# Kernel tuning notes

Hardware: AMD Instinct MI355X
Metric: run time of the kernel (lower is better)

Reference implementation:

```python
import jax, jax.numpy as jnp
import numpy as np

B, S, D, H, O, E = 2, 2048, 1024, 2048, 1024, 8


def setup_inputs() -> dict:
    key = jax.random.key(0)
    k_x, k_rw, k_w1, k_w3, k_w2 = jax.random.split(key, 5)
    sD = 1.0 / np.sqrt(D)
    sH = 1.0 / np.sqrt(H)
    return {
        "x": jax.random.normal(k_x, (B, S, D), dtype=jnp.float32),
        "router_w": jax.random.normal(k_rw, (E, D), dtype=jnp.float32) * sD,  # nn.Linear(D, E).weight
        "router_b": jnp.zeros((E,), dtype=jnp.float32),
        "W1": jax.random.normal(k_w1, (E, D, H), dtype=jnp.float32) * sD,  # per-expert w1 (x @ W1)
        "W3": jax.random.normal(k_w3, (E, D, H), dtype=jnp.float32) * sD,  # per-expert gate w3
        "W2": jax.random.normal(k_w2, (E, H, O), dtype=jnp.float32) * sH,  # per-expert down-proj
        "top_k": 2,
    }


def reference(x, router_w, router_b, W1, W3, W2, top_k):
    b, s, d = x.shape
    xf = x.reshape(-1, d)  # [T, D], T = B*S
    T = xf.shape[0]

    # Router: softmax over experts, then top-k and renormalize
    logits = xf @ router_w.T + router_b            # [T, E]
    probs = jax.nn.softmax(logits, axis=-1)
    top_p, top_i = jax.lax.top_k(probs, top_k)     # [T, k]
    top_p = top_p / top_p.sum(axis=-1, keepdims=True)

    # Dense all-expert SwiGLU MLPs (faithful to reference: every expert on every token)
    h = jnp.einsum('td,edh->eth', xf, W1)          # [E, T, H]
    g = jnp.einsum('td,edh->eth', xf, W3)          # [E, T, H]
    eo = jnp.einsum('eth,eho->eto', jax.nn.silu(h) * g, W2)  # [E, T, O]

    # Gather each token's top-k expert outputs and combine
    sel = eo[top_i, jnp.arange(T)[:, None]]        # [T, k, O]
    out = jnp.sum(top_p[..., None] * sel, axis=1)  # [T, O]
    return out.reshape(b, s, -1)
```

## Files before the change

kernel.cpp:

```cpp
#include <hip/hip_runtime.h>
#include <hip/hip_bf16.h>

#define TTOK 4096
#define DIM  1024
#define HID  2048
#define ODIM 1024
#define NE   8

typedef __attribute__((ext_vector_type(8))) short  short8;
typedef __attribute__((ext_vector_type(4))) float  f32x4;
typedef __attribute__((ext_vector_type(8))) unsigned short ushort8;

#define WAITVM(N) asm volatile("s_waitcnt vmcnt(" #N ")" ::: "memory")
#define BAR() __builtin_amdgcn_s_barrier()

__device__ __forceinline__ unsigned short f2bf(float f){
  unsigned u = __float_as_uint(f);
  u += 0x7fffu + ((u >> 16) & 1u);
  return (unsigned short)(u >> 16);
}

__device__ __forceinline__ void gld16(const void* g, void* l){
  __builtin_amdgcn_global_load_lds(
      (const __attribute__((address_space(1))) unsigned int*)g,
      (__attribute__((address_space(3))) unsigned int*)l, 16, 0, 0);
}

__global__ __launch_bounds__(256) void router_kernel(
    const float* __restrict__ x, const float* __restrict__ rw,
    const float* __restrict__ rb, unsigned short* __restrict__ xbf,
    int2* __restrict__ toke, float2* __restrict__ tokw)
{
  int tok  = (blockIdx.x * blockDim.x + threadIdx.x) >> 6;
  int lane = threadIdx.x & 63;
  const float4* xr = (const float4*)(x + (size_t)tok * DIM + lane * 16);
  float xv[16];
#pragma unroll
  for (int q = 0; q < 4; q++){
    float4 v = xr[q];
    xv[q*4+0]=v.x; xv[q*4+1]=v.y; xv[q*4+2]=v.z; xv[q*4+3]=v.w;
  }
  ushort8 u0, u1;
#pragma unroll
  for (int j = 0; j < 8; j++){ u0[j] = f2bf(xv[j]); u1[j] = f2bf(xv[8+j]); }
  ushort8* xo = (ushort8*)(xbf + (size_t)tok * DIM + lane * 16);
  xo[0] = u0; xo[1] = u1;

  float lg[NE];
#pragma unroll
  for (int e = 0; e < NE; e++){
    const float4* wr4 = (const float4*)(rw + (size_t)e * DIM + lane * 16);
    float s = 0.f;
#pragma unroll
    for (int q = 0; q < 4; q++){
      float4 wv = wr4[q];
      s += xv[q*4+0]*wv.x + xv[q*4+1]*wv.y + xv[q*4+2]*wv.z + xv[q*4+3]*wv.w;
    }
    lg[e] = s;
  }
#pragma unroll
  for (int e = 0; e < NE; e++)
    for (int s = 1; s < 64; s <<= 1) lg[e] += __shfl_xor(lg[e], s, 64);

  if (lane == 0){
#pragma unroll
    for (int e = 0; e < NE; e++) lg[e] += rb[e];
    int e0 = 0; float l0 = lg[0];
    for (int e = 1; e < NE; e++) if (lg[e] > l0){ l0 = lg[e]; e0 = e; }
    int e1 = -1; float l1 = -1e30f;
    for (int e = 0; e < NE; e++) if (e != e0 && lg[e] > l1){ l1 = lg[e]; e1 = e; }
    float w0 = 1.f / (1.f + __expf(l1 - l0));
    float w1 = 1.f / (1.f + __expf(l0 - l1));
    toke[tok] = make_int2(e0, e1);
    tokw[tok] = make_float2(w0, w1);
  }
}

__global__ __launch_bounds__(256) void plan_kernel(
    const int2* __restrict__ toke, const float2* __restrict__ tokw,
    int* __restrict__ counts, int* __restrict__ offs,
    int* __restrict__ tlist, float* __restrict__ wlist)
{
  const int e  = blockIdx.x;
  const int t  = threadIdx.x;
  const int lane = t & 63, wv = t >> 6;
  __shared__ int sh[4 * 8];
  __shared__ int tot[8];
  __shared__ int sw[4];

  int wcnt[NE];
#pragma unroll
  for (int ee = 0; ee < NE; ee++) wcnt[ee] = 0;
  for (int base = 0; base < TTOK; base += 256){
    int2 p = toke[base + t];
#pragma unroll
    for (int ee = 0; ee < NE; ee++){
      unsigned long long m = __ballot(p.x == ee || p.y == ee);
      if (lane == 0) wcnt[ee] += __popcll(m);
    }
  }
  if (lane == 0){
#pragma unroll
    for (int ee = 0; ee < NE; ee++) sh[wv * 8 + ee] = wcnt[ee];
  }
  __syncthreads();
  if (t < NE) tot[t] = sh[t] + sh[8 + t] + sh[16 + t] + sh[24 + t];
  __syncthreads();

  int my_off = 0;
#pragma unroll
  for (int ee = 0; ee < NE; ee++) if (ee < e) my_off += tot[ee];

  if (e == 0 && t < NE){
    counts[t] = tot[t];
    int o = 0;
    for (int ee = 0; ee < NE; ee++){ if (ee < t) o += tot[ee]; }
    offs[t] = o;
    if (t == 0){
      int s = 0;
      for (int ee = 0; ee < NE; ee++) s += tot[ee];
      offs[NE] = s;
    }
  }

  int running = my_off;
  for (int base = 0; base < TTOK; base += 256){
    int tokid = base + t;
    int2  p = toke[tokid];
    float2 wgt = tokw[tokid];
    bool s0 = (p.x == e), s1 = (p.y == e);
    bool flag = s0 || s1;
    unsigned long long m = __ballot(flag);
    int rank_in_wave = __popcll(m & ((lane == 0) ? 0ull : ((~0ull) >> (64 - lane))));
    if (lane == 0) sw[wv] = __popcll(m);
    __syncthreads();
    int wave_base = 0, tot4 = 0;
#pragma unroll
    for (int w2 = 0; w2 < 4; w2++){ int v = sw[w2]; tot4 += v; if (w2 < wv) wave_base += v; }
    if (flag){
      int pos = running + wave_base + rank_in_wave;
      tlist[pos] = tokid;
      wlist[pos] = s0 ? wgt.x : wgt.y;
    }
    running += tot4;
    __syncthreads();
  }
}

__global__ __launch_bounds__(256) void transpose_cvt(
    const float* __restrict__ in, unsigned short* __restrict__ out, int R, int C)
{
  __shared__ __align__(16) unsigned short tl[64 * 128];
  int e = blockIdx.z;
  const float* src = in + (size_t)e * R * C + (size_t)(blockIdx.y * 128) * C + blockIdx.x * 64;
  unsigned short* dst = out + (size_t)e * C * R + (size_t)(blockIdx.x * 64) * R + blockIdx.y * 128;
  int t = threadIdx.x;
#pragma unroll
  for (int i = 0; i < 8; i++){
    int idx = i * 256 + t;
    int c = idx & 63, r0 = (idx >> 6) * 4;
    unsigned short v[4];
#pragma unroll
    for (int j = 0; j < 4; j++) v[j] = f2bf(src[(size_t)(r0 + j) * C + c]);
    unsigned long long pk = (unsigned long long)v[0] | ((unsigned long long)v[1] << 16)
      | ((unsigned long long)v[2] << 32) | ((unsigned long long)v[3] << 48);
    *(unsigned long long*)((char*)tl + c * 256 + (((r0 >> 3) ^ (c & 15)) * 16) + (r0 & 7) * 2) = pk;
  }
  __syncthreads();
#pragma unroll
  for (int i = 0; i < 4; i++){
    int idx = i * 256 + t;
    int c = idx >> 4, r0 = (idx & 15) * 8;
    ushort8 u = *(const ushort8*)((const char*)tl + c * 256 + (((r0 >> 3) ^ (c & 15)) * 16));
    *(ushort8*)(dst + (size_t)c * R + r0) = u;
  }
}

__global__ __launch_bounds__(256,2) void ffn1_kernel(
    const unsigned short* __restrict__ xbf,
    const unsigned short* __restrict__ w1t,
    const unsigned short* __restrict__ w3t,
    unsigned short* __restrict__ abuf,
    const int* __restrict__ counts, const int* __restrict__ offs,
    const int* __restrict__ tlist)
{
  const int wgid = blockIdx.x;
  const int e = wgid & 7;
  const int j = wgid >> 3;
  const int u = j & 15, g = j >> 4;
  const int ct = (g & 7) * 2 + (u >> 3);
  const int rt = (g >> 3) * 8 + (u & 7);
  const int cnt = counts[e];
  const int rbase = rt * 128;
  if (rbase >= cnt) return;
  const int off = offs[e];
  const int rows_left = cnt - rbase;
  const int t = threadIdx.x;
  const int lane = t & 63, w = t >> 6;
  const int wr = w >> 1, wc = w & 1;

  __shared__ __align__(16) unsigned short lds[2 * 12288];

  int ar0 = t >> 2, ar1 = 64 + (t >> 2);
  int psw = (t & 3) ^ ((t >> 3) & 3);
  int ra0 = ar0 < rows_left ? ar0 : rows_left - 1;
  int ra1 = ar1 < rows_left ? ar1 : rows_left - 1;
  int tok0 = tlist[off + rbase + ra0];
  int tok1 = tlist[off + rbase + ra1];
  const char* sA0  = (const char*)xbf + ((size_t)tok0 * DIM) * 2 + psw * 16;
  const char* sA1  = (const char*)xbf + ((size_t)tok1 * DIM) * 2 + psw * 16;
  const char* sB10 = (const char*)w1t + (((size_t)e * HID + ct * 128 + ar0) * DIM) * 2 + psw * 16;
  const char* sB11 = (const char*)w1t + (((size_t)e * HID + ct * 128 + ar1) * DIM) * 2 + psw * 16;
  const char* sB30 = (const char*)w3t + (((size_t)e * HID + ct * 128 + ar0) * DIM) * 2 + psw * 16;
  const char* sB31 = (const char*)w3t + (((size_t)e * HID + ct * 128 + ar1) * DIM) * 2 + psw * 16;
  const int dofs = w * 1024;

  auto STAGE = [&](int bs, int kt){
    int kb = kt << 6;
    char* base = (char*)lds + bs * 24576;
    gld16(sA0  + kb, base +            dofs);
    gld16(sA1  + kb, base +  4096 +    dofs);
    gld16(sB10 + kb, base +  8192 +    dofs);
    gld16(sB11 + kb, base + 12288 +    dofs);
    gld16(sB30 + kb, base + 16384 +    dofs);
    gld16(sB31 + kb, base + 20480 +    dofs);
  };

  const int chsw = ((lane >> 4) ^ ((lane >> 1) & 3)) * 8;
  int aofs[4], b1ofs[4], b3ofs[4];
#pragma unroll
  for (int i = 0; i < 4; i++){
    int am = wr * 64 + i * 16 + (lane & 15);
    int bn = wc * 64 + i * 16 + (lane & 15);
    aofs[i]  = am * 32 + chsw;
    b1ofs[i] = 4096 + bn * 32 + chsw;
    b3ofs[i] = 8192 + bn * 32 + chsw;
  }

  f32x4 acch[4][4], accg[4][4];
#pragma unroll
  for (int i = 0; i < 4; i++)
#pragma unroll
    for (int jj = 0; jj < 4; jj++){
      acch[i][jj] = (f32x4){0.f,0.f,0.f,0.f};
      accg[i][jj] = (f32x4){0.f,0.f,0.f,0.f};
    }

  auto COMPUTE = [&](int bs){
    const unsigned short* L = lds + bs * 12288;
    short8 a[4], b1[4], b3[4];
#pragma unroll
    for (int i = 0; i < 4; i++){
      a[i]  = *(const short8*)(L + aofs[i]);
      b1[i] = *(const short8*)(L + b1ofs[i]);
      b3[i] = *(const short8*)(L + b3ofs[i]);
    }
    __builtin_amdgcn_s_setprio(1);
#pragma unroll
    for (int mi = 0; mi < 4; mi++)
#pragma unroll
      for (int ni = 0; ni < 4; ni++){
        acch[mi][ni] = __builtin_amdgcn_mfma_f32_16x16x32_bf16(a[mi], b1[ni], acch[mi][ni], 0, 0, 0);
        accg[mi][ni] = __builtin_amdgcn_mfma_f32_16x16x32_bf16(a[mi], b3[ni], accg[mi][ni], 0, 0, 0);
      }
    __builtin_amdgcn_s_setprio(0);
  };

  STAGE(0, 0);
  int kt = 0;
  for (; kt < DIM / 32 - 1; ++kt){
    STAGE((kt + 1) & 1, kt + 1);
    WAITVM(6); BAR();
    COMPUTE(kt & 1);
    BAR();
  }
  WAITVM(0); BAR();
  COMPUTE(kt & 1);

#pragma unroll
  for (int mi = 0; mi < 4; mi++)
#pragma unroll
    for (int r = 0; r < 4; r++){
      int row_local = wr * 64 + mi * 16 + ((lane >> 4) << 2) + r;
      if (row_local < rows_left){
        size_t pair = (size_t)(off + rbase + row_local);
        unsigned short* arow = abuf + pair * HID + ct * 128 + wc * 64 + (lane & 15);
#pragma unroll
        for (int ni = 0; ni < 4; ni++){
          float h = acch[mi][ni][r], gg = accg[mi][ni][r];
          float sv = h / (1.f + __expf(-h));
          arow[ni * 16] = f2bf(sv * gg);
        }
      }
    }
}

__global__ __launch_bounds__(256,3) void ffn2_kernel(
    const unsigned short* __restrict__ abuf,
    const unsigned short* __restrict__ w2t,
    float* __restrict__ dout,
    const int* __restrict__ counts, const int* __restrict__ offs,
    const int* __restrict__ tlist, const float* __restrict__ wlist)
{
  const int wgid = blockIdx.x;
  const int e = wgid & 7;
  const int j = wgid >> 3;
  const int u = j & 7, g = j >> 3;
  const int ct = (g & 3) * 2 + (u >> 2);
  const int rt = (g >> 2) * 4 + (u & 3);
  const int cnt = counts[e];
  const int rbase = rt * 128;
  if (rbase >= cnt) return;
  const int off = offs[e];
  const int rows_left = cnt - rbase;
  const int t = threadIdx.x;
  const int lane = t & 63, w = t >> 6;
  const int wr = w >> 1, wc = w & 1;

  __shared__ __align__(16) unsigned short lds[2 * 8192];

  int ar0 = t >> 2, ar1 = 64 + (t >> 2);
  int psw = (t & 3) ^ ((t >> 3) & 3);
  int ra0 = ar0 < rows_left ? ar0 : rows_left - 1;
  int ra1 = ar1 < rows_left ? ar1 : rows_left - 1;
  const char* sA0 = (const char*)abuf + ((size_t)(off + rbase + ra0) * HID) * 2 + psw * 16;
  const char* sA1 = (const char*)abuf + ((size_t)(off + rbase + ra1) * HID) * 2 + psw * 16;
  const char* sB0 = (const char*)w2t + (((size_t)e * ODIM + ct * 128 + ar0) * HID) * 2 + psw * 16;
  const char* sB1 = (const char*)w2t + (((size_t)e * ODIM + ct * 128 + ar1) * HID) * 2 + psw * 16;
  const int dofs = w * 1024;

  auto STAGE = [&](int bs, int kt){
    int kb = kt << 6;
    char* base = (char*)lds + bs * 16384;
    gld16(sA0 + kb, base +           dofs);
    gld16(sA1 + kb, base +  4096 +   dofs);
    gld16(sB0 + kb, base +  8192 +   dofs);
    gld16(sB1 + kb, base + 12288 +   dofs);
  };

  const int chsw = ((lane >> 4) ^ ((lane >> 1) & 3)) * 8;
  int aofs[4], bofs[4];
#pragma unroll
  for (int i = 0; i < 4; i++){
    int am = wr * 64 + i * 16 + (lane & 15);
    int bn = wc * 64 + i * 16 + (lane & 15);
    aofs[i] = am * 32 + chsw;
    bofs[i] = 4096 + bn * 32 + chsw;
  }

  f32x4 acc[4][4];
#pragma unroll
  for (int i = 0; i < 4; i++)
#pragma unroll
    for (int jj = 0; jj < 4; jj++) acc[i][jj] = (f32x4){0.f,0.f,0.f,0.f};

  auto COMPUTE = [&](int bs){
    const unsigned short* L = lds + bs * 8192;
    short8 a[4], b[4];
#pragma unroll
    for (int i = 0; i < 4; i++){
      a[i] = *(const short8*)(L + aofs[i]);
      b[i] = *(const short8*)(L + bofs[i]);
    }
    __builtin_amdgcn_s_setprio(1);
#pragma unroll
    for (int mi = 0; mi < 4; mi++)
#pragma unroll
      for (int ni = 0; ni < 4; ni++)
        acc[mi][ni] = __builtin_amdgcn_mfma_f32_16x16x32_bf16(a[mi], b[ni], acc[mi][ni], 0, 0, 0);
    __builtin_amdgcn_s_setprio(0);
  };

  STAGE(0, 0);
  int kt = 0;
  for (; kt < HID / 32 - 1; ++kt){
    STAGE((kt + 1) & 1, kt + 1);
    WAITVM(4); BAR();
    COMPUTE(kt & 1);
    BAR();
  }
  WAITVM(0); BAR();
  COMPUTE(kt & 1);

#pragma unroll
  for (int mi = 0; mi < 4; mi++)
#pragma unroll
    for (int r = 0; r < 4; r++){
      int row_local = wr * 64 + mi * 16 + ((lane >> 4) << 2) + r;
      if (row_local < rows_left){
        int pair = off + rbase + row_local;
        int token = tlist[pair];
        float p   = wlist[pair];
        float* orow = dout + (size_t)token * ODIM + ct * 128 + wc * 64 + (lane & 15);
#pragma unroll
        for (int ni = 0; ni < 4; ni++)
          atomicAdd(orow + ni * 16, p * acc[mi][ni][r]);
      }
    }
}

extern "C" void kernel_launch(void* const* d_in, const int* in_sizes, int n_in,
                              void* d_out, int out_size, void* d_ws, size_t ws_size,
                              hipStream_t stream)
{
  const float* x  = (const float*)d_in[0];
  const float* rw = (const float*)d_in[1];
  const float* rb = (const float*)d_in[2];
  const float* W1 = (const float*)d_in[3];
  const float* W3 = (const float*)d_in[4];
  const float* W2 = (const float*)d_in[5];

  char* ws = (char*)d_ws;
  const size_t off_ctrl = 0;
  const size_t off_toke = 256;
  const size_t off_tokw = off_toke + (size_t)TTOK * 8;
  const size_t off_tl   = off_tokw + (size_t)TTOK * 8;
  const size_t off_wl   = off_tl   + (size_t)2 * TTOK * 4;
  const size_t off_xbf  = off_wl   + (size_t)2 * TTOK * 4;
  const size_t off_w1t  = off_xbf  + (size_t)TTOK * DIM * 2;
  const size_t off_w3t  = off_w1t  + (size_t)NE * HID * DIM * 2;
  const size_t off_w2t  = off_w3t  + (size_t)NE * HID * DIM * 2;
  const size_t off_ab   = off_w2t  + (size_t)NE * ODIM * HID * 2;
  const size_t need     = off_ab   + (size_t)2 * TTOK * HID * 2;
  if (ws_size < need) return;

  int* counts = (int*)(ws + off_ctrl);
  int* offs   = (int*)(ws + off_ctrl + 64);
  int2*   toke = (int2*)  (ws + off_toke);
  float2* tokw = (float2*)(ws + off_tokw);
  int*    tl   = (int*)   (ws + off_tl);
  float*  wl   = (float*) (ws + off_wl);
  unsigned short* xbf = (unsigned short*)(ws + off_xbf);
  unsigned short* w1t = (unsigned short*)(ws + off_w1t);
  unsigned short* w3t = (unsigned short*)(ws + off_w3t);
  unsigned short* w2t = (unsigned short*)(ws + off_w2t);
  unsigned short* ab  = (unsigned short*)(ws + off_ab);

  hipMemsetAsync(d_out, 0, (size_t)out_size * sizeof(float), stream);

  router_kernel<<<TTOK / 4, 256, 0, stream>>>(x, rw, rb, xbf, toke, tokw);
  plan_kernel<<<NE, 256, 0, stream>>>(toke, tokw, counts, offs, tl, wl);

  transpose_cvt<<<dim3(HID / 64, DIM / 128, NE), 256, 0, stream>>>(W1, w1t, DIM, HID);
  transpose_cvt<<<dim3(HID / 64, DIM / 128, NE), 256, 0, stream>>>(W3, w3t, DIM, HID);
  transpose_cvt<<<dim3(ODIM / 64, HID / 128, NE), 256, 0, stream>>>(W2, w2t, HID, ODIM);

  ffn1_kernel<<<NE * 16 * 32, 256, 0, stream>>>(xbf, w1t, w3t, ab, counts, offs, tl);
  ffn2_kernel<<<NE * 8 * 32, 256, 0, stream>>>(ab, w2t, (float*)d_out, counts, offs, tl, wl);
}
```

Measured before the change: 262.5 us.

## Interleave W1/W3 weights and enlarge FFN GEMM tiles to 256x256 with 8 waves

W1 and W3 are transposed into one interleaved buffer (16-column groups alternating), so the gate and up projections run as a single GEMM with one B operand stream. Both FFN kernels move from 128x128 tiles with 4 waves to 256x256 tiles with 8 waves, a K step of 64 split into two halves, and a finer-grained LDS double-buffer schedule that interleaves loads with half-tile MFMA batches. The aim is more data reuse per LDS load and fewer redundant A reads. In exchange it uses 128KB of LDS per block and more accumulator registers, and the larger tiles leave fewer blocks and coarser padding for the uneven per-expert token counts.

```diff
diff --git a/kernel.cpp b/kernel.cpp
--- a/kernel.cpp
+++ b/kernel.cpp
@@ -148,12 +148,12 @@
 }
 
 __global__ __launch_bounds__(256) void transpose_cvt(
-    const float* __restrict__ in, unsigned short* __restrict__ out, int R, int C)
+    const float* __restrict__ in, unsigned short* __restrict__ out,
+    int R, int C, int ilv, size_t ostride)
 {
   __shared__ __align__(16) unsigned short tl[64 * 128];
   int e = blockIdx.z;
   const float* src = in + (size_t)e * R * C + (size_t)(blockIdx.y * 128) * C + blockIdx.x * 64;
-  unsigned short* dst = out + (size_t)e * C * R + (size_t)(blockIdx.x * 64) * R + blockIdx.y * 128;
   int t = threadIdx.x;
 #pragma unroll
   for (int i = 0; i < 8; i++){
@@ -172,14 +172,16 @@
     int idx = i * 256 + t;
     int c = idx >> 4, r0 = (idx & 15) * 8;
     ushort8 u = *(const ushort8*)((const char*)tl + c * 256 + (((r0 >> 3) ^ (c & 15)) * 16));
-    *(ushort8*)(dst + (size_t)c * R + r0) = u;
-  }
-}
-
-__global__ __launch_bounds__(256,2) void ffn1_kernel(
+    int cg = blockIdx.x * 64 + c;
+    int q  = (ilv < 0) ? cg : (((cg >> 4) << 5) + ilv + (cg & 15));
+    *(ushort8*)(out + (size_t)e * ostride + (size_t)q * R + blockIdx.y * 128 + r0) = u;
+  }
+}
+
+
+__global__ __launch_bounds__(512,2) void ffn1_kernel(
     const unsigned short* __restrict__ xbf,
-    const unsigned short* __restrict__ w1t,
-    const unsigned short* __restrict__ w3t,
+    const unsigned short* __restrict__ wcat,
     unsigned short* __restrict__ abuf,
     const int* __restrict__ counts, const int* __restrict__ offs,
     const int* __restrict__ tlist)
@@ -187,115 +189,109 @@
   const int wgid = blockIdx.x;
   const int e = wgid & 7;
   const int j = wgid >> 3;
-  const int u = j & 15, g = j >> 4;
-  const int ct = (g & 7) * 2 + (u >> 3);
-  const int rt = (g >> 3) * 8 + (u & 7);
+  const int ct = j & 15;
+  const int rt = j >> 4;
   const int cnt = counts[e];
-  const int rbase = rt * 128;
+  const int rbase = rt * 256;
   if (rbase >= cnt) return;
   const int off = offs[e];
   const int rows_left = cnt - rbase;
   const int t = threadIdx.x;
-  const int lane = t & 63, w = t >> 6;
-  const int wr = w >> 1, wc = w & 1;
-
-  __shared__ __align__(16) unsigned short lds[2 * 12288];
-
-  int ar0 = t >> 2, ar1 = 64 + (t >> 2);
-  int psw = (t & 3) ^ ((t >> 3) & 3);
-  int ra0 = ar0 < rows_left ? ar0 : rows_left - 1;
-  int ra1 = ar1 < rows_left ? ar1 : rows_left - 1;
-  int tok0 = tlist[off + rbase + ra0];
-  int tok1 = tlist[off + rbase + ra1];
-  const char* sA0  = (const char*)xbf + ((size_t)tok0 * DIM) * 2 + psw * 16;
-  const char* sA1  = (const char*)xbf + ((size_t)tok1 * DIM) * 2 + psw * 16;
-  const char* sB10 = (const char*)w1t + (((size_t)e * HID + ct * 128 + ar0) * DIM) * 2 + psw * 16;
-  const char* sB11 = (const char*)w1t + (((size_t)e * HID + ct * 128 + ar1) * DIM) * 2 + psw * 16;
-  const char* sB30 = (const char*)w3t + (((size_t)e * HID + ct * 128 + ar0) * DIM) * 2 + psw * 16;
-  const char* sB31 = (const char*)w3t + (((size_t)e * HID + ct * 128 + ar1) * DIM) * 2 + psw * 16;
-  const int dofs = w * 1024;
-
-  auto STAGE = [&](int bs, int kt){
-    int kb = kt << 6;
-    char* base = (char*)lds + bs * 24576;
-    gld16(sA0  + kb, base +            dofs);
-    gld16(sA1  + kb, base +  4096 +    dofs);
-    gld16(sB10 + kb, base +  8192 +    dofs);
-    gld16(sB11 + kb, base + 12288 +    dofs);
-    gld16(sB30 + kb, base + 16384 +    dofs);
-    gld16(sB31 + kb, base + 20480 +    dofs);
-  };
-
-  const int chsw = ((lane >> 4) ^ ((lane >> 1) & 3)) * 8;
-  int aofs[4], b1ofs[4], b3ofs[4];
-#pragma unroll
-  for (int i = 0; i < 4; i++){
-    int am = wr * 64 + i * 16 + (lane & 15);
-    int bn = wc * 64 + i * 16 + (lane & 15);
-    aofs[i]  = am * 32 + chsw;
-    b1ofs[i] = 4096 + bn * 32 + chsw;
-    b3ofs[i] = 8192 + bn * 32 + chsw;
-  }
-
-  f32x4 acch[4][4], accg[4][4];
-#pragma unroll
-  for (int i = 0; i < 4; i++)
-#pragma unroll
-    for (int jj = 0; jj < 4; jj++){
-      acch[i][jj] = (f32x4){0.f,0.f,0.f,0.f};
-      accg[i][jj] = (f32x4){0.f,0.f,0.f,0.f};
-    }
-
-  auto COMPUTE = [&](int bs){
-    const unsigned short* L = lds + bs * 12288;
-    short8 a[4], b1[4], b3[4];
-#pragma unroll
-    for (int i = 0; i < 4; i++){
-      a[i]  = *(const short8*)(L + aofs[i]);
-      b1[i] = *(const short8*)(L + b1ofs[i]);
-      b3[i] = *(const short8*)(L + b3ofs[i]);
-    }
+  const int l = t & 63, w = t >> 6;
+  const int wr = w >> 2, wc = w & 3;
+
+  __shared__ __align__(16) unsigned short lds[2 * 32768];
+
+  const int R0 = 32 * w + (l >> 2), R1 = R0 + 16;
+  const int csrc = ((l & 3) ^ ((l >> 3) & 3)) * 16;
+  int raa0 = R0 < rows_left ? R0 : rows_left - 1;
+  int raa1 = R1 < rows_left ? R1 : rows_left - 1;
+  const char* pA0 = (const char*)xbf + (size_t)tlist[off + rbase + raa0] * 2048 + csrc;
+  const char* pA1 = (const char*)xbf + (size_t)tlist[off + rbase + raa1] * 2048 + csrc;
+  const char* pB0 = (const char*)wcat + ((size_t)e * 4096 + ct * 256 + R0) * 2048 + csrc;
+  const char* pB1 = (const char*)wcat + ((size_t)e * 4096 + ct * 256 + R1) * 2048 + csrc;
+
+  auto STA = [&](int bs, int kt, int kk){
+    char* d = (char*)lds + bs * 65536 + kk * 16384 + (2 * w) * 1024;
+    int o = kt * 128 + kk * 64;
+    gld16(pA0 + o, d); gld16(pA1 + o, d + 1024);
+  };
+  auto STB = [&](int bs, int kt, int kk){
+    char* d = (char*)lds + bs * 65536 + 32768 + kk * 16384 + (2 * w) * 1024;
+    int o = kt * 128 + kk * 64;
+    gld16(pB0 + o, d); gld16(pB1 + o, d + 1024);
+  };
+
+  const int chsw = ((l >> 4) ^ ((l >> 1) & 3)) * 8;
+  int aro[8], bro[4];
+#pragma unroll
+  for (int mi = 0; mi < 8; mi++) aro[mi] = (wr * 128 + mi * 16 + (l & 15)) * 32 + chsw;
+#pragma unroll
+  for (int ni = 0; ni < 4; ni++) bro[ni] = (wc * 64 + ni * 16 + (l & 15)) * 32 + chsw;
+
+  f32x4 acc[8][4];
+#pragma unroll
+  for (int i = 0; i < 8; i++)
+#pragma unroll
+    for (int jj = 0; jj < 4; jj++) acc[i][jj] = (f32x4){0.f,0.f,0.f,0.f};
+
+  short8 a[4], b[4];
+  auto LDA = [&](int bs, int kk, int mih){
+    const unsigned short* L = lds + bs * 32768 + kk * 8192;
+#pragma unroll
+    for (int i = 0; i < 4; i++) a[i] = *(const short8*)(L + aro[mih * 4 + i]);
+  };
+  auto LDB = [&](int bs, int kk){
+    const unsigned short* L = lds + bs * 32768 + 16384 + kk * 8192;
+#pragma unroll
+    for (int i = 0; i < 4; i++) b[i] = *(const short8*)(L + bro[i]);
+  };
+  auto MQ = [&](int mih){
     __builtin_amdgcn_s_setprio(1);
 #pragma unroll
-    for (int mi = 0; mi < 4; mi++)
-#pragma unroll
-      for (int ni = 0; ni < 4; ni++){
-        acch[mi][ni] = __builtin_amdgcn_mfma_f32_16x16x32_bf16(a[mi], b1[ni], acch[mi][ni], 0, 0, 0);
-        accg[mi][ni] = __builtin_amdgcn_mfma_f32_16x16x32_bf16(a[mi], b3[ni], accg[mi][ni], 0, 0, 0);
-      }
+    for (int m4 = 0; m4 < 4; m4++)
+#pragma unroll
+      for (int ni = 0; ni < 4; ni++)
+        acc[mih * 4 + m4][ni] = __builtin_amdgcn_mfma_f32_16x16x32_bf16(a[m4], b[ni], acc[mih * 4 + m4][ni], 0, 0, 0);
     __builtin_amdgcn_s_setprio(0);
   };
 
-  STAGE(0, 0);
-  int kt = 0;
-  for (; kt < DIM / 32 - 1; ++kt){
-    STAGE((kt + 1) & 1, kt + 1);
-    WAITVM(6); BAR();
-    COMPUTE(kt & 1);
-    BAR();
-  }
+  const int NK = DIM / 64;
+  STA(0, 0, 0); STB(0, 0, 0); STA(0, 0, 1); STB(0, 0, 1);
   WAITVM(0); BAR();
-  COMPUTE(kt & 1);
-
-#pragma unroll
-  for (int mi = 0; mi < 4; mi++)
+
+  for (int kt = 0; kt < NK - 1; ++kt){
+    const int bs = kt & 1, nb = bs ^ 1;
+    LDA(bs,0,0); LDB(bs,0); STA(nb,kt+1,0);            BAR(); MQ(0); BAR();
+    LDA(bs,0,1);            STB(nb,kt+1,0); WAITVM(4); BAR(); MQ(1); BAR();
+    LDA(bs,1,0); LDB(bs,1); STA(nb,kt+1,1);            BAR(); MQ(0); BAR();
+    LDA(bs,1,1);            STB(nb,kt+1,1); WAITVM(4); BAR(); MQ(1); BAR();
+  }
+  {
+    const int bs = (NK - 1) & 1;
+    LDA(bs,0,0); LDB(bs,0);            BAR(); MQ(0); BAR();
+    LDA(bs,0,1);            WAITVM(0); BAR(); MQ(1); BAR();
+    LDA(bs,1,0); LDB(bs,1);            BAR(); MQ(0); BAR();
+    LDA(bs,1,1);                       BAR(); MQ(1);
+  }
+
+#pragma unroll
+  for (int mi = 0; mi < 8; mi++)
 #pragma unroll
     for (int r = 0; r < 4; r++){
-      int row_local = wr * 64 + mi * 16 + ((lane >> 4) << 2) + r;
+      int row_local = wr * 128 + mi * 16 + ((l >> 4) << 2) + r;
       if (row_local < rows_left){
         size_t pair = (size_t)(off + rbase + row_local);
-        unsigned short* arow = abuf + pair * HID + ct * 128 + wc * 64 + (lane & 15);
-#pragma unroll
-        for (int ni = 0; ni < 4; ni++){
-          float h = acch[mi][ni][r], gg = accg[mi][ni][r];
-          float sv = h / (1.f + __expf(-h));
-          arow[ni * 16] = f2bf(sv * gg);
-        }
+        unsigned short* arow = abuf + pair * HID + ct * 128 + wc * 32 + (l & 15);
+        float h0 = acc[mi][0][r], g0 = acc[mi][1][r];
+        arow[0]  = f2bf((h0 / (1.f + __expf(-h0))) * g0);
+        float h1 = acc[mi][2][r], g1 = acc[mi][3][r];
+        arow[16] = f2bf((h1 / (1.f + __expf(-h1))) * g1);
       }
     }
 }
 
-__global__ __launch_bounds__(256,3) void ffn2_kernel(
+__global__ __launch_bounds__(512,2) void ffn2_kernel(
     const unsigned short* __restrict__ abuf,
     const unsigned short* __restrict__ w2t,
     float* __restrict__ dout,
@@ -305,93 +301,102 @@
   const int wgid = blockIdx.x;
   const int e = wgid & 7;
   const int j = wgid >> 3;
-  const int u = j & 7, g = j >> 3;
-  const int ct = (g & 3) * 2 + (u >> 2);
-  const int rt = (g >> 2) * 4 + (u & 3);
+  const int ct = j & 3;
+  const int rt = j >> 2;
   const int cnt = counts[e];
-  const int rbase = rt * 128;
+  const int rbase = rt * 256;
   if (rbase >= cnt) return;
   const int off = offs[e];
   const int rows_left = cnt - rbase;
   const int t = threadIdx.x;
-  const int lane = t & 63, w = t >> 6;
-  const int wr = w >> 1, wc = w & 1;
-
-  __shared__ __align__(16) unsigned short lds[2 * 8192];
-
-  int ar0 = t >> 2, ar1 = 64 + (t >> 2);
-  int psw = (t & 3) ^ ((t >> 3) & 3);
-  int ra0 = ar0 < rows_left ? ar0 : rows_left - 1;
-  int ra1 = ar1 < rows_left ? ar1 : rows_left - 1;
-  const char* sA0 = (const char*)abuf + ((size_t)(off + rbase + ra0) * HID) * 2 + psw * 16;
-  const char* sA1 = (const char*)abuf + ((size_t)(off + rbase + ra1) * HID) * 2 + psw * 16;
-  const char* sB0 = (const char*)w2t + (((size_t)e * ODIM + ct * 128 + ar0) * HID) * 2 + psw * 16;
-  const char* sB1 = (const char*)w2t + (((size_t)e * ODIM + ct * 128 + ar1) * HID) * 2 + psw * 16;
-  const int dofs = w * 1024;
-
-  auto STAGE = [&](int bs, int kt){
-    int kb = kt << 6;
-    char* base = (char*)lds + bs * 16384;
-    gld16(sA0 + kb, base +           dofs);
-    gld16(sA1 + kb, base +  4096 +   dofs);
-    gld16(sB0 + kb, base +  8192 +   dofs);
-    gld16(sB1 + kb, base + 12288 +   dofs);
-  };
-
-  const int chsw = ((lane >> 4) ^ ((lane >> 1) & 3)) * 8;
-  int aofs[4], bofs[4];
-#pragma unroll
-  for (int i = 0; i < 4; i++){
-    int am = wr * 64 + i * 16 + (lane & 15);
-    int bn = wc * 64 + i * 16 + (lane & 15);
-    aofs[i] = am * 32 + chsw;
-    bofs[i] = 4096 + bn * 32 + chsw;
-  }
-
-  f32x4 acc[4][4];
-#pragma unroll
-  for (int i = 0; i < 4; i++)
+  const int l = t & 63, w = t >> 6;
+  const int wr = w >> 2, wc = w & 3;
+
+  __shared__ __align__(16) unsigned short lds[2 * 32768];
+
+  const int R0 = 32 * w + (l >> 2), R1 = R0 + 16;
+  const int csrc = ((l & 3) ^ ((l >> 3) & 3)) * 16;
+  int raa0 = R0 < rows_left ? R0 : rows_left - 1;
+  int raa1 = R1 < rows_left ? R1 : rows_left - 1;
+  const char* pA0 = (const char*)abuf + (size_t)(off + rbase + raa0) * 4096 + csrc;
+  const char* pA1 = (const char*)abuf + (size_t)(off + rbase + raa1) * 4096 + csrc;
+  const char* pB0 = (const char*)w2t + ((size_t)e * 1024 + ct * 256 + R0) * 4096 + csrc;
+  const char* pB1 = (const char*)w2t + ((size_t)e * 1024 + ct * 256 + R1) * 4096 + csrc;
+
+  auto STA = [&](int bs, int kt, int kk){
+    char* d = (char*)lds + bs * 65536 + kk * 16384 + (2 * w) * 1024;
+    int o = kt * 128 + kk * 64;
+    gld16(pA0 + o, d); gld16(pA1 + o, d + 1024);
+  };
+  auto STB = [&](int bs, int kt, int kk){
+    char* d = (char*)lds + bs * 65536 + 32768 + kk * 16384 + (2 * w) * 1024;
+    int o = kt * 128 + kk * 64;
+    gld16(pB0 + o, d); gld16(pB1 + o, d + 1024);
+  };
+
+  const int chsw = ((l >> 4) ^ ((l >> 1) & 3)) * 8;
+  int aro[8], bro[4];
+#pragma unroll
+  for (int mi = 0; mi < 8; mi++) aro[mi] = (wr * 128 + mi * 16 + (l & 15)) * 32 + chsw;
+#pragma unroll
+  for (int ni = 0; ni < 4; ni++) bro[ni] = (wc * 64 + ni * 16 + (l & 15)) * 32 + chsw;
+
+  f32x4 acc[8][4];
+#pragma unroll
+  for (int i = 0; i < 8; i++)
 #pragma unroll
     for (int jj = 0; jj < 4; jj++) acc[i][jj] = (f32x4){0.f,0.f,0.f,0.f};
 
-  auto COMPUTE = [&](int bs){
-    const unsigned short* L = lds + bs * 8192;
-    short8 a[4], b[4];
-#pragma unroll
-    for (int i = 0; i < 4; i++){
-      a[i] = *(const short8*)(L + aofs[i]);
-      b[i] = *(const short8*)(L + bofs[i]);
-    }
+  short8 a[4], b[4];
+  auto LDA = [&](int bs, int kk, int mih){
+    const unsigned short* L = lds + bs * 32768 + kk * 8192;
+#pragma unroll
+    for (int i = 0; i < 4; i++) a[i] = *(const short8*)(L + aro[mih * 4 + i]);
+  };
+  auto LDB = [&](int bs, int kk){
+    const unsigned short* L = lds + bs * 32768 + 16384 + kk * 8192;
+#pragma unroll
+    for (int i = 0; i < 4; i++) b[i] = *(const short8*)(L + bro[i]);
+  };
+  auto MQ = [&](int mih){
     __builtin_amdgcn_s_setprio(1);
 #pragma unroll
-    for (int mi = 0; mi < 4; mi++)
+    for (int m4 = 0; m4 < 4; m4++)
 #pragma unroll
       for (int ni = 0; ni < 4; ni++)
-        acc[mi][ni] = __builtin_amdgcn_mfma_f32_16x16x32_bf16(a[mi], b[ni], acc[mi][ni], 0, 0, 0);
+        acc[mih * 4 + m4][ni] = __builtin_amdgcn_mfma_f32_16x16x32_bf16(a[m4], b[ni], acc[mih * 4 + m4][ni], 0, 0, 0);
     __builtin_amdgcn_s_setprio(0);
   };
 
-  STAGE(0, 0);
-  int kt = 0;
-  for (; kt < HID / 32 - 1; ++kt){
-    STAGE((kt + 1) & 1, kt + 1);
-    WAITVM(4); BAR();
-    COMPUTE(kt & 1);
-    BAR();
-  }
+  const int NK = HID / 64;
+  STA(0, 0, 0); STB(0, 0, 0); STA(0, 0, 1); STB(0, 0, 1);
   WAITVM(0); BAR();
-  COMPUTE(kt & 1);
-
-#pragma unroll
-  for (int mi = 0; mi < 4; mi++)
+
+  for (int kt = 0; kt < NK - 1; ++kt){
+    const int bs = kt & 1, nb = bs ^ 1;
+    LDA(bs,0,0); LDB(bs,0); STA(nb,kt+1,0);            BAR(); MQ(0); BAR();
+    LDA(bs,0,1);            STB(nb,kt+1,0); WAITVM(4); BAR(); MQ(1); BAR();
+    LDA(bs,1,0); LDB(bs,1); STA(nb,kt+1,1);            BAR(); MQ(0); BAR();
+    LDA(bs,1,1);            STB(nb,kt+1,1); WAITVM(4); BAR(); MQ(1); BAR();
+  }
+  {
+    const int bs = (NK - 1) & 1;
+    LDA(bs,0,0); LDB(bs,0);            BAR(); MQ(0); BAR();
+    LDA(bs,0,1);            WAITVM(0); BAR(); MQ(1); BAR();
+    LDA(bs,1,0); LDB(bs,1);            BAR(); MQ(0); BAR();
+    LDA(bs,1,1);                       BAR(); MQ(1);
+  }
+
+#pragma unroll
+  for (int mi = 0; mi < 8; mi++)
 #pragma unroll
     for (int r = 0; r < 4; r++){
-      int row_local = wr * 64 + mi * 16 + ((lane >> 4) << 2) + r;
+      int row_local = wr * 128 + mi * 16 + ((l >> 4) << 2) + r;
       if (row_local < rows_left){
         int pair = off + rbase + row_local;
         int token = tlist[pair];
         float p   = wlist[pair];
-        float* orow = dout + (size_t)token * ODIM + ct * 128 + wc * 64 + (lane & 15);
+        float* orow = dout + (size_t)token * ODIM + ct * 256 + wc * 64 + (l & 15);
 #pragma unroll
         for (int ni = 0; ni < 4; ni++)
           atomicAdd(orow + ni * 16, p * acc[mi][ni][r]);
@@ -417,9 +422,8 @@
   const size_t off_tl   = off_tokw + (size_t)TTOK * 8;
   const size_t off_wl   = off_tl   + (size_t)2 * TTOK * 4;
   const size_t off_xbf  = off_wl   + (size_t)2 * TTOK * 4;
-  const size_t off_w1t  = off_xbf  + (size_t)TTOK * DIM * 2;
-  const size_t off_w3t  = off_w1t  + (size_t)NE * HID * DIM * 2;
-  const size_t off_w2t  = off_w3t  + (size_t)NE * HID * DIM * 2;
+  const size_t off_wcat = off_xbf  + (size_t)TTOK * DIM * 2;
+  const size_t off_w2t  = off_wcat + (size_t)NE * 2 * HID * DIM * 2;
   const size_t off_ab   = off_w2t  + (size_t)NE * ODIM * HID * 2;
   const size_t need     = off_ab   + (size_t)2 * TTOK * HID * 2;
   if (ws_size < need) return;
@@ -430,21 +434,20 @@
   float2* tokw = (float2*)(ws + off_tokw);
   int*    tl   = (int*)   (ws + off_tl);
   float*  wl   = (float*) (ws + off_wl);
-  unsigned short* xbf = (unsigned short*)(ws + off_xbf);
-  unsigned short* w1t = (unsigned short*)(ws + off_w1t);
-  unsigned short* w3t = (unsigned short*)(ws + off_w3t);
-  unsigned short* w2t = (unsigned short*)(ws + off_w2t);
-  unsigned short* ab  = (unsigned short*)(ws + off_ab);
+  unsigned short* xbf  = (unsigned short*)(ws + off_xbf);
+  unsigned short* wcat = (unsigned short*)(ws + off_wcat);
+  unsigned short* w2t  = (unsigned short*)(ws + off_w2t);
+  unsigned short* ab   = (unsigned short*)(ws + off_ab);
 
   hipMemsetAsync(d_out, 0, (size_t)out_size * sizeof(float), stream);
 
   router_kernel<<<TTOK / 4, 256, 0, stream>>>(x, rw, rb, xbf, toke, tokw);
   plan_kernel<<<NE, 256, 0, stream>>>(toke, tokw, counts, offs, tl, wl);
 
-  transpose_cvt<<<dim3(HID / 64, DIM / 128, NE), 256, 0, stream>>>(W1, w1t, DIM, HID);
-  transpose_cvt<<<dim3(HID / 64, DIM / 128, NE), 256, 0, stream>>>(W3, w3t, DIM, HID);
-  transpose_cvt<<<dim3(ODIM / 64, HID / 128, NE), 256, 0, stream>>>(W2, w2t, HID, ODIM);
-
-  ffn1_kernel<<<NE * 16 * 32, 256, 0, stream>>>(xbf, w1t, w3t, ab, counts, offs, tl);
-  ffn2_kernel<<<NE * 8 * 32, 256, 0, stream>>>(ab, w2t, (float*)d_out, counts, offs, tl, wl);
-}
+  transpose_cvt<<<dim3(HID / 64, DIM / 128, NE), 256, 0, stream>>>(W1, wcat, DIM, HID, 0,  (size_t)2 * HID * DIM);
+  transpose_cvt<<<dim3(HID / 64, DIM / 128, NE), 256, 0, stream>>>(W3, wcat, DIM, HID, 16, (size_t)2 * HID * DIM);
+  transpose_cvt<<<dim3(ODIM / 64, HID / 128, NE), 256, 0, stream>>>(W2, w2t, HID, ODIM, -1, (size_t)ODIM * HID);
+
+  ffn1_kernel<<<NE * 16 * 16, 512, 0, stream>>>(xbf, wcat, ab, counts, offs, tl);
+  ffn2_kernel<<<NE * 4 * 16, 512, 0, stream>>>(ab, w2t, (float*)d_out, counts, offs, tl, wl);
+}
```

Result: slower. 269.6 us (+2.7%).
